# Optimization experiments

Hardware: AMD Instinct MI355X
Metric: run time of the kernel (lower is better)

## Reference

```python
import jax, jax.numpy as jnp
import numpy as np

N_GROUPS = 32  # getGroupSize(.) assumed -> channels // 8 (or //24 for 3*ch) == 32 for ch=256
HEADS = 4


def group_norm(x, gamma, beta, groups=N_GROUPS, eps=1e-5):
    n, c = x.shape
    xg = x.reshape(n, groups, c // groups)
    mu = xg.mean(-1, keepdims=True)
    var = xg.var(-1, keepdims=True)
    xn = ((xg - mu) * jax.lax.rsqrt(var + eps)).reshape(n, c)
    return xn * gamma + beta


def setup_inputs():
    key = jax.random.key(0)
    N, E, CH, HID = 2000, 16000, 256, 256
    ks = jax.random.split(key, 24)

    def w(k, shape, s=0.02):
        return (jax.random.normal(k, shape) * s).astype(jnp.float32)

    inp = {
        'x': jax.random.normal(ks[0], (N, CH), jnp.float32),
        'edge_index': jax.random.randint(ks[1], (2, E), 0, N),
        'edge_attr': jax.random.normal(ks[2], (E, CH), jnp.float32),
        # edge_mlp: GN(3ch)+ReLU -> Linear(3ch,hid) -> GN(hid)+ReLU -> Linear(hid,ch)
        'gn_e1_g': jnp.ones((3 * CH,), jnp.float32), 'gn_e1_b': jnp.zeros((3 * CH,), jnp.float32),
        'We1': w(ks[3], (3 * CH, HID)), 'be1': jnp.zeros((HID,), jnp.float32),
        'gn_e2_g': jnp.ones((HID,), jnp.float32), 'gn_e2_b': jnp.zeros((HID,), jnp.float32),
        'We2': w(ks[4], (HID, CH)), 'be2': jnp.zeros((CH,), jnp.float32),
        # actN: GN(ch)+ReLU
        'gn_n_g': jnp.ones((CH,), jnp.float32), 'gn_n_b': jnp.zeros((CH,), jnp.float32),
        # multi-head attention projections
        'Wq': w(ks[5], (CH, CH)), 'bq': jnp.zeros((CH,), jnp.float32),
        'Wk': w(ks[6], (CH, CH)), 'bk': jnp.zeros((CH,), jnp.float32),
        'Wv': w(ks[7], (CH, CH)), 'bv': jnp.zeros((CH,), jnp.float32),
        'Wo': w(ks[8], (CH, CH)), 'bo': jnp.zeros((CH,), jnp.float32),
        # node_mlp: Linear(2ch,hid) -> GN(hid)+ReLU -> Linear(hid,ch)
        'Wn1': w(ks[9], (2 * CH, HID)), 'bn1': jnp.zeros((HID,), jnp.float32),
        'gn_n2_g': jnp.ones((HID,), jnp.float32), 'gn_n2_b': jnp.zeros((HID,), jnp.float32),
        'Wn2': w(ks[10], (HID, CH)), 'bn2': jnp.zeros((CH,), jnp.float32),
    }
    return inp


def reference(x, edge_index, edge_attr,
              gn_e1_g, gn_e1_b, We1, be1, gn_e2_g, gn_e2_b, We2, be2,
              gn_n_g, gn_n_b, Wq, bq, Wk, bk, Wv, bv, Wo, bo,
              Wn1, bn1, gn_n2_g, gn_n2_b, Wn2, bn2):
    row, col = edge_index[0], edge_index[1]
    N, ch = x.shape
    E = edge_attr.shape[0]
    dk = ch // HEADS

    # ---- edge model: cat(src, tgt, e) -> GN/ReLU -> Lin -> GN/ReLU -> Lin (+res) ----
    e_in = jnp.concatenate([x[row], x[col], edge_attr], axis=1)  # [E, 3ch]
    h = jax.nn.relu(group_norm(e_in, gn_e1_g, gn_e1_b))
    h = h @ We1 + be1
    h = jax.nn.relu(group_norm(h, gn_e2_g, gn_e2_b))
    e_out = h @ We2 + be2 + edge_attr  # [E, ch]

    # ---- node model: dense-masked MHA, queries=nodes, keys/values=edges ----
    mask = jnp.zeros((N, E), x.dtype).at[col, jnp.arange(E)].set(1.0)  # scatter adjacency
    q = (x @ Wq + bq).reshape(N, HEADS, dk)
    k = (e_out @ Wk + bk).reshape(E, HEADS, dk)
    v = (e_out @ Wv + bv).reshape(E, HEADS, dk)
    scores = jnp.einsum('nhd,ehd->hne', q, k) / jnp.sqrt(jnp.float32(dk))  # [H, N, E]
    scores = jnp.where(mask[None] > 0, scores, jnp.float32(-1e9))
    attn = jax.nn.softmax(scores, axis=-1)
    g = jnp.einsum('hne,ehd->nhd', attn, v).reshape(N, ch) @ Wo + bo  # [N, ch]

    xa = jax.nn.relu(group_norm(x, gn_n_g, gn_n_b))
    h = jnp.concatenate([xa, g], axis=1) @ Wn1 + bn1  # thinker='cat'
    h = jax.nn.relu(group_norm(h, gn_n2_g, gn_n2_b))
    n_out = h @ Wn2 + bn2 + x  # residual

    return n_out, e_out
```

## Files before the change

### kernel.cpp

```cpp
#include <hip/hip_runtime.h>
#include <hip/hip_bf16.h>
#include <stdint.h>
#include <math.h>

#define CH 256

typedef __attribute__((ext_vector_type(8)))  short short8;
typedef __attribute__((ext_vector_type(16))) short short16;
typedef __attribute__((ext_vector_type(4)))  float f32x4;

#define GL2LDS16(g, l) __builtin_amdgcn_global_load_lds(                       \
    (const __attribute__((address_space(1))) void*)(g),                        \
    (__attribute__((address_space(3))) void*)(l), 16, 0, 0)

__device__ inline short f2bf(float f) {
    __hip_bfloat16 h = __float2bfloat16(f);
    short s;
    __builtin_memcpy(&s, &h, 2);
    return s;
}

__device__ inline float bf2f(short s) {
    unsigned u = ((unsigned)(unsigned short)s) << 16;
    float f;
    __builtin_memcpy(&f, &u, 4);
    return f;
}

__device__ inline float warp_sum64(float v) {
    v += __shfl_xor(v, 32, 64);
    v += __shfl_xor(v, 16, 64);
    v += __shfl_xor(v, 8, 64);
    v += __shfl_xor(v, 4, 64);
    v += __shfl_xor(v, 2, 64);
    v += __shfl_xor(v, 1, 64);
    return v;
}

__device__ inline float warp_max64(float v) {
    v = fmaxf(v, __shfl_xor(v, 32, 64));
    v = fmaxf(v, __shfl_xor(v, 16, 64));
    v = fmaxf(v, __shfl_xor(v, 8, 64));
    v = fmaxf(v, __shfl_xor(v, 4, 64));
    v = fmaxf(v, __shfl_xor(v, 2, 64));
    v = fmaxf(v, __shfl_xor(v, 1, 64));
    return v;
}

struct GArgs {
    const short* A; const short* Bt; const float* bias; const float* res;
    float* C; short* Cbf;
    const float* gamma; const float* beta; float* vbar;
    int M, K, Nc, ldc, coff;
    const short* A2; const short* Bt2; const float* bias2; short* Cbf2;
    int M2, Nc2, y_split;
    const int* coli;
    int* cursor; int* elist;
    const int* counts; int* offsets; int Nn;
};

template <int BM, int BN, int EPI, int DUAL, int VB, int FILL,
          int SCAN = 0, int PAN2 = 0, int XSWZ = 0>
__global__ __launch_bounds__(256) void mfma_gemm(GArgs g)
{
    constexpr int BK = 64;
    constexpr int HM = BM / 2, HN = BN / 2;
    constexpr int FM = HM / 16, FN = HN / 16;
    constexpr int PA = BM / 32;
    constexpr int PB = BN / 32;
    constexpr int NP2 = PAN2 ? 2 : 1;
    __shared__ short As[BM * BK];
    __shared__ short Bs[NP2 * BN * BK];

    const short* A = g.A; const short* Bt = g.Bt;
    const float* bias = g.bias; const float* res = g.res;
    float* C = g.C; short* Cbf = g.Cbf;
    int M = g.M, ldc = g.ldc, co = g.coff;
    const int K = g.K;
    int by = blockIdx.y, bx = blockIdx.x;

    if constexpr (SCAN) {
        if (by == (int)gridDim.y - 1) {
            const int t0 = threadIdx.x;
            if (bx == 0) {
                int* ss = (int*)As;
                int base8 = t0 * 8;
                int loc[8]; int srun = 0;
                #pragma unroll
                for (int j = 0; j < 8; j++) {
                    int idx = base8 + j;
                    int c = (idx < g.Nn) ? g.counts[idx] : 0;
                    loc[j] = srun; srun += c;
                }
                ss[t0] = srun;
                __syncthreads();
                for (int off = 1; off < 256; off <<= 1) {
                    int v = (t0 >= off) ? ss[t0 - off] : 0;
                    __syncthreads();
                    ss[t0] += v;
                    __syncthreads();
                }
                int excl = (t0 > 0) ? ss[t0 - 1] : 0;
                #pragma unroll
                for (int j = 0; j < 8; j++) {
                    int idx = base8 + j;
                    if (idx < g.Nn) {
                        int v = excl + loc[j];
                        g.offsets[idx] = v;
                        g.cursor[idx]  = v;
                    }
                }
                if (t0 == 255) g.offsets[g.Nn] = ss[255];
            }
            return;
        }
    }

    bool qrole = false;
    if constexpr (DUAL) {
        if (by >= g.y_split) {
            by -= g.y_split;
            if (bx * BN >= g.Nc2) return;
            qrole = true;
            A = g.A2; Bt = g.Bt2; bias = g.bias2; Cbf = g.Cbf2;
            C = nullptr; res = nullptr;
            M = g.M2; ldc = g.Nc2; co = 0;
        }
    }

    if constexpr (XSWZ) {
        if (!qrole) {
            int h = by * 4 + bx;
            int lby = (h >> 5) * 8 + (h & 7);
            if (lby * BM >= M) return;
            by = lby;
            bx = (h >> 3) & 3;
        }
    }

    const int t = threadIdx.x;
    const int wave = t >> 6, lane = t & 63;
    const int q = lane >> 4, l16 = lane & 15;
    const int row0 = by * BM;
    const int col0 = bx * BN;
    const int wm = wave & 1, wn = wave >> 1;

    if constexpr (FILL) {
        if (!qrole && bx == 0 && t < BM) {
            int rg = row0 + t;
            if (rg < M) {
                int c = g.coli[rg];
                int p = atomicAdd(&g.cursor[c], 1);
                g.elist[p] = rg;
            }
        }
    }

    f32x4 acc[NP2][FM][FN];
    #pragma unroll
    for (int p2 = 0; p2 < NP2; p2++)
        #pragma unroll
        for (int i = 0; i < FM; i++)
            #pragma unroll
            for (int j = 0; j < FN; j++) acc[p2][i][j] = (f32x4){0.f, 0.f, 0.f, 0.f};

    for (int k0 = 0; k0 < K; k0 += BK) {
        #pragma unroll
        for (int p = 0; p < PA; p++) {
            int chunk = p * 256 + t;
            int r = chunk >> 3;
            int cs = (((chunk & 7) ^ (r & 7)) * 8);
            int gr = row0 + r; if (gr >= M) gr = M - 1;
            const short* gsrc = A + (size_t)gr * K + k0 + cs;
            short* ldst = &As[(p * 256 + wave * 64) * 8];
            GL2LDS16(gsrc, ldst);
        }
        #pragma unroll
        for (int p2 = 0; p2 < NP2; p2++) {
            if (!(PAN2 && p2 == 1 && qrole)) {
                #pragma unroll
                for (int p = 0; p < PB; p++) {
                    int chunk = p * 256 + t;
                    int r = chunk >> 3;
                    int cs = (((chunk & 7) ^ (r & 7)) * 8);
                    const short* gsrc = Bt + (size_t)(col0 + p2 * 256 + r) * K + k0 + cs;
                    short* ldst = &Bs[p2 * BN * BK + (p * 256 + wave * 64) * 8];
                    GL2LDS16(gsrc, ldst);
                }
            }
        }
        __syncthreads();
        #pragma unroll
        for (int ks = 0; ks < 2; ks++) {
            short8 af[FM];
            #pragma unroll
            for (int mi = 0; mi < FM; mi++) {
                int R = wm * HM + mi * 16 + l16;
                int slot = ((ks * 4 + q) ^ (R & 7)) * 8;
                af[mi] = *(const short8*)&As[R * BK + slot];
            }
            #pragma unroll
            for (int p2 = 0; p2 < NP2; p2++) {
                if (!(PAN2 && p2 == 1 && qrole)) {
                    short8 bfr[FN];
                    #pragma unroll
                    for (int ni = 0; ni < FN; ni++) {
                        int R = wn * HN + ni * 16 + l16;
                        int slot = ((ks * 4 + q) ^ (R & 7)) * 8;
                        bfr[ni] = *(const short8*)&Bs[p2 * BN * BK + R * BK + slot];
                    }
                    #pragma unroll
                    for (int mi = 0; mi < FM; mi++)
                        #pragma unroll
                        for (int ni = 0; ni < FN; ni++)
                            acc[p2][mi][ni] = __builtin_amdgcn_mfma_f32_16x16x32_bf16(
                                af[mi], bfr[ni], acc[p2][mi][ni], 0, 0, 0);
                }
            }
        }
        __syncthreads();
    }

    #pragma unroll
    for (int p2 = 0; p2 < NP2; p2++) {
        if (PAN2 && p2 == 1 && qrole) continue;
        #pragma unroll
        for (int ni = 0; ni < FN; ni++) {
            int cg = col0 + p2 * 256 + wn * HN + ni * 16 + l16;
            float bv = bias[cg];
            if constexpr (EPI == 1) {
                float ga = g.gamma[cg], be = g.beta[cg];
                #pragma unroll
                for (int mi = 0; mi < FM; mi++) {
                    #pragma unroll
                    for (int r = 0; r < 4; r++) {
                        float v = acc[p2][mi][ni][r] + bv;
                        float s = v, sq = v * v;
                        s += __shfl_xor(s, 1, 64);  sq += __shfl_xor(sq, 1, 64);
                        s += __shfl_xor(s, 2, 64);  sq += __shfl_xor(sq, 2, 64);
                        s += __shfl_xor(s, 4, 64);  sq += __shfl_xor(sq, 4, 64);
                        float mean = s * 0.125f;
                        float var = sq * 0.125f - mean * mean;
                        float o = fmaxf((v - mean) * rsqrtf(var + 1e-5f) * ga + be, 0.f);
                        int rg = row0 + wm * HM + mi * 16 + q * 4 + r;
                        if (rg < M) Cbf[(size_t)rg * ldc + co + cg] = f2bf(o);
                    }
                }
            } else {
                #pragma unroll
                for (int mi = 0; mi < FM; mi++) {
                    #pragma unroll
                    for (int r = 0; r < 4; r++) {
                        int rg = row0 + wm * HM + mi * 16 + q * 4 + r;
                        if (rg < M) {
                            float v = acc[p2][mi][ni][r] + bv;
                            if (res) v += res[(size_t)rg * ldc + co + cg];
                            if (C)   C[(size_t)rg * ldc + co + cg] = v;
                            if (Cbf) Cbf[(size_t)rg * ldc + co + cg] = f2bf(v);
                        }
                    }
                }
                if constexpr (VB) {
                    bool vpanel = PAN2 ? (p2 == 1) : (!qrole && cg >= 256);
                    if (vpanel) {
                        float part = 0.f;
                        #pragma unroll
                        for (int mi = 0; mi < FM; mi++)
                            #pragma unroll
                            for (int r = 0; r < 4; r++) {
                                int rg = row0 + wm * HM + mi * 16 + q * 4 + r;
                                if (rg < M) part += acc[p2][mi][ni][r] + bv;
                            }
                        part += __shfl_xor(part, 16, 64);
                        part += __shfl_xor(part, 32, 64);
                        if (q == 0) atomicAdd(&g.vbar[cg - 256], part);
                    }
                }
            }
        }
    }
}

struct PrepPack {
    const float* wsrc[7];
    short* wdst[7];
    int wK[7];
    int wE[7];
    int wstart[7];
    int NW, NF, NP;
    const float* Wo; const float* Wn1s; const float* bo; const float* bn1;
    short* Wn1t; float* b2f;
    const float* x;
    short* x_bf;
    short* cat_bf;
    float2* xs;
    const float* gng;
    const float* gnb;
    float* vbar;
    const float* bk;
    const float* bv;
    float* bkv;
    int* counts;
    int N;
};

__global__ __launch_bounds__(256) void prep_kernel(PrepPack p)
{
    int bid = blockIdx.x;
    int t = threadIdx.x;
    if (bid < p.NW) {
        int m = 0;
        #pragma unroll
        for (int i = 1; i < 7; i++) if (bid >= p.wstart[i]) m = i;
        int k0 = (bid - p.wstart[m]) * 16;
        const float* src = p.wsrc[m];
        short16 o;
        #pragma unroll
        for (int j = 0; j < 16; j++) o[j] = f2bf(src[(size_t)(k0 + j) * 256 + t]);
        *(short16*)(p.wdst[m] + (size_t)t * p.wK[m] + k0) = o;
        return;
    }
    if (bid < p.NW + p.NF) {
        int c = bid - p.NW;
        __shared__ float colv[256];
        __shared__ float red[4];
        colv[t] = p.Wn1s[(size_t)(256 + t) * 256 + c];
        __syncthreads();
        const float* wrow = p.Wo + (size_t)t * 256;
        float acc = 0.f;
        #pragma unroll 4
        for (int j = 0; j < 256; j++) acc += wrow[j] * colv[j];
        p.Wn1t[(size_t)c * 512 + 256 + t] = f2bf(acc);
        float bvp = p.bo[t] * colv[t];
        bvp = warp_sum64(bvp);
        if ((t & 63) == 0) red[t >> 6] = bvp;
        __syncthreads();
        if (t == 0) p.b2f[c] = p.bn1[c] + red[0] + red[1] + red[2] + red[3];
        return;
    }
    if (bid >= p.NW + p.NF + p.NP) {
        int i = (bid - p.NW - p.NF - p.NP) * 256 + t;
        if (i < p.N) p.counts[i] = 0;
        return;
    }
    int pb = bid - p.NW - p.NF;
    if (pb == 0) {
        p.vbar[t] = 0.f;
        p.bkv[t] = p.bk[t];
        p.bkv[256 + t] = p.bv[t];
    }
    int r = pb * 8 + (t >> 5);
    int g = t & 31;
    if (r >= p.N) return;
    size_t xb = (size_t)r * CH + g * 8;
    float4 a = *(const float4*)&p.x[xb];
    float4 b = *(const float4*)&p.x[xb + 4];
    short8 xr;
    xr[0] = f2bf(a.x); xr[1] = f2bf(a.y); xr[2] = f2bf(a.z); xr[3] = f2bf(a.w);
    xr[4] = f2bf(b.x); xr[5] = f2bf(b.y); xr[6] = f2bf(b.z); xr[7] = f2bf(b.w);
    *(short8*)&p.x_bf[xb] = xr;
    float s  = a.x + a.y + a.z + a.w + b.x + b.y + b.z + b.w;
    float s2 = a.x*a.x + a.y*a.y + a.z*a.z + a.w*a.w
             + b.x*b.x + b.y*b.y + b.z*b.z + b.w*b.w;
    p.xs[(size_t)r * 32 + g] = make_float2(s, s2);
    float m = s * 0.125f;
    float var = s2 * 0.125f - m * m;
    float rsd = rsqrtf(var + 1e-5f);
    float4 g0 = *(const float4*)&p.gng[g * 8];
    float4 g1 = *(const float4*)&p.gng[g * 8 + 4];
    float4 b0 = *(const float4*)&p.gnb[g * 8];
    float4 b1 = *(const float4*)&p.gnb[g * 8 + 4];
    short8 o;
    o[0] = f2bf(fmaxf((a.x - m) * rsd * g0.x + b0.x, 0.f));
    o[1] = f2bf(fmaxf((a.y - m) * rsd * g0.y + b0.y, 0.f));
    o[2] = f2bf(fmaxf((a.z - m) * rsd * g0.z + b0.z, 0.f));
    o[3] = f2bf(fmaxf((a.w - m) * rsd * g0.w + b0.w, 0.f));
    o[4] = f2bf(fmaxf((b.x - m) * rsd * g1.x + b1.x, 0.f));
    o[5] = f2bf(fmaxf((b.y - m) * rsd * g1.y + b1.y, 0.f));
    o[6] = f2bf(fmaxf((b.z - m) * rsd * g1.z + b1.z, 0.f));
    o[7] = f2bf(fmaxf((b.w - m) * rsd * g1.w + b1.w, 0.f));
    *(short8*)&p.cat_bf[(size_t)r * (2 * CH) + g * 8] = o;
}

__global__ __launch_bounds__(256) void estats_kernel(
    const float* __restrict__ eattr, const int* __restrict__ rowi,
    const int* __restrict__ coli, const float2* __restrict__ xs,
    const short* __restrict__ x_bf,
    const float* __restrict__ g1v, const float* __restrict__ b1v,
    short* __restrict__ e1n, int* __restrict__ counts, int E)
{
    __shared__ float2 ea[8][32];
    __shared__ float2 musr[8][32];
    int t = threadIdx.x;
    int slot = t >> 5, g = t & 31;
    int e = blockIdx.x * 8 + slot;
    float4 a = *(const float4*)&eattr[(size_t)e * CH + g * 8];
    float4 b = *(const float4*)&eattr[(size_t)e * CH + g * 8 + 4];
    float s  = a.x + a.y + a.z + a.w + b.x + b.y + b.z + b.w;
    float s2 = a.x*a.x + a.y*a.y + a.z*a.z + a.w*a.w
             + b.x*b.x + b.y*b.y + b.z*b.z + b.w*b.w;
    ea[slot][g] = make_float2(s, s2);
    int r = rowi[e], c = coli[e];
    if (g == 0) atomicAdd(&counts[c], 1);
    __syncthreads();
    float S = 0.f, S2 = 0.f;
    #pragma unroll
    for (int j = 0; j < 3; j++) {
        int b3 = 3 * g + j;
        int src = b3 >> 5, idx = b3 & 31;
        float2 v;
        if (src == 0)      v = xs[(size_t)r * 32 + idx];
        else if (src == 1) v = xs[(size_t)c * 32 + idx];
        else               v = ea[slot][idx];
        S += v.x; S2 += v.y;
    }
    float m = S * (1.f / 24.f);
    float var = S2 * (1.f / 24.f) - m * m;
    musr[slot][g] = make_float2(m, rsqrtf(var + 1e-5f));
    __syncthreads();
    #pragma unroll
    for (int seg = 0; seg < 3; seg++) {
        int pos = seg * 256 + g * 8;
        float2 ms = musr[slot][pos / 24];
        float4 ga  = *(const float4*)&g1v[pos];
        float4 ga2 = *(const float4*)&g1v[pos + 4];
        float4 gb  = *(const float4*)&b1v[pos];
        float4 gb2 = *(const float4*)&b1v[pos + 4];
        float v0, v1, v2, v3, v4, v5, v6, v7;
        if (seg == 2) {
            v0 = a.x; v1 = a.y; v2 = a.z; v3 = a.w;
            v4 = b.x; v5 = b.y; v6 = b.z; v7 = b.w;
        } else {
            const short* srow = x_bf + (size_t)(seg == 0 ? r : c) * CH + g * 8;
            short8 v8 = *(const short8*)srow;
            v0 = bf2f(v8[0]); v1 = bf2f(v8[1]); v2 = bf2f(v8[2]); v3 = bf2f(v8[3]);
            v4 = bf2f(v8[4]); v5 = bf2f(v8[5]); v6 = bf2f(v8[6]); v7 = bf2f(v8[7]);
        }
        short8 o;
        o[0] = f2bf(fmaxf((v0 - ms.x) * ms.y * ga.x  + gb.x,  0.f));
        o[1] = f2bf(fmaxf((v1 - ms.x) * ms.y * ga.y  + gb.y,  0.f));
        o[2] = f2bf(fmaxf((v2 - ms.x) * ms.y * ga.z  + gb.z,  0.f));
        o[3] = f2bf(fmaxf((v3 - ms.x) * ms.y * ga.w  + gb.w,  0.f));
        o[4] = f2bf(fmaxf((v4 - ms.x) * ms.y * ga2.x + gb2.x, 0.f));
        o[5] = f2bf(fmaxf((v5 - ms.x) * ms.y * ga2.y + gb2.y, 0.f));
        o[6] = f2bf(fmaxf((v6 - ms.x) * ms.y * ga2.z + gb2.z, 0.f));
        o[7] = f2bf(fmaxf((v7 - ms.x) * ms.y * ga2.w + gb2.w, 0.f));
        *(short8*)&e1n[(size_t)e * 768 + pos] = o;
    }
}

__global__ __launch_bounds__(256) void attn_kernel(
    const short* __restrict__ qb, const short* __restrict__ kvb,
    const int* __restrict__ offsets, const int* __restrict__ elist,
    const float* __restrict__ vbar, short* __restrict__ gout, int N, int E)
{
    __shared__ int eidx[64];
    __shared__ float scl[4 * 64];
    int n = blockIdx.x;
    int wave = threadIdx.x >> 6;
    int lane = threadIdx.x & 63;
    int s0 = offsets[n], s1 = offsets[n + 1];
    float q0 = bf2f(qb[(size_t)n * CH + lane]);
    float q1 = bf2f(qb[(size_t)n * CH + 64 + lane]);
    float q2 = bf2f(qb[(size_t)n * CH + 128 + lane]);
    float q3 = bf2f(qb[(size_t)n * CH + 192 + lane]);
    float out = 0.f, m = -INFINITY, l = 0.f;
    for (int base = s0; base < s1; base += 64) {
        int cn = s1 - base; if (cn > 64) cn = 64;
        if (wave == 0 && lane < cn) eidx[lane] = elist[base + lane];
        __syncthreads();
        for (int j = wave; j < cn; j += 4) {
            int e = eidx[j];
            const short* kr = kvb + (size_t)e * 512;
            float d0 = warp_sum64(q0 * bf2f(kr[lane]));
            float d1 = warp_sum64(q1 * bf2f(kr[64 + lane]));
            float d2 = warp_sum64(q2 * bf2f(kr[128 + lane]));
            float d3 = warp_sum64(q3 * bf2f(kr[192 + lane]));
            if (lane == 0) {
                scl[j]       = d0 * 0.125f;
                scl[64 + j]  = d1 * 0.125f;
                scl[128 + j] = d2 * 0.125f;
                scl[192 + j] = d3 * 0.125f;
            }
        }
        __syncthreads();
        float s = (lane < cn) ? scl[wave * 64 + lane] : -INFINITY;
        float mc = warp_max64(s);
        float nm = fmaxf(m, mc);
        float scale = __expf(m - nm);
        float pp = (lane < cn) ? __expf(s - nm) : 0.f;
        float ps = warp_sum64(pp);
        l = l * scale + ps;
        out *= scale;
        m = nm;
        for (int i = 0; i < cn; i++) {
            float pi = __shfl(pp, i, 64);
            int ei = eidx[i];
            out += pi * bf2f(kvb[(size_t)ei * 512 + 256 + wave * 64 + lane]);
        }
        __syncthreads();
    }
    float res;
    if (s1 > s0) res = out / l;
    else         res = vbar[wave * 64 + lane] * (1.f / (float)E);
    gout[(size_t)n * 512 + wave * 64 + lane] = f2bf(res);
}

extern "C" void kernel_launch(void* const* d_in, const int* in_sizes, int n_in,
                              void* d_out, int out_size, void* d_ws, size_t ws_size,
                              hipStream_t stream)
{
    const float* x       = (const float*)d_in[0];
    const int*   ei      = (const int*)d_in[1];
    const float* eattr   = (const float*)d_in[2];
    const float* gn_e1_g = (const float*)d_in[3];
    const float* gn_e1_b = (const float*)d_in[4];
    const float* We1     = (const float*)d_in[5];
    const float* be1     = (const float*)d_in[6];
    const float* gn_e2_g = (const float*)d_in[7];
    const float* gn_e2_b = (const float*)d_in[8];
    const float* We2     = (const float*)d_in[9];
    const float* be2     = (const float*)d_in[10];
    const float* gn_n_g  = (const float*)d_in[11];
    const float* gn_n_b  = (const float*)d_in[12];
    const float* Wq      = (const float*)d_in[13];
    const float* bq      = (const float*)d_in[14];
    const float* Wk      = (const float*)d_in[15];
    const float* bk      = (const float*)d_in[16];
    const float* Wv      = (const float*)d_in[17];
    const float* bv      = (const float*)d_in[18];
    const float* Wo      = (const float*)d_in[19];
    const float* bo      = (const float*)d_in[20];
    const float* Wn1     = (const float*)d_in[21];
    const float* bn1     = (const float*)d_in[22];
    const float* gn_n2_g = (const float*)d_in[23];
    const float* gn_n2_b = (const float*)d_in[24];
    const float* Wn2     = (const float*)d_in[25];
    const float* bn2     = (const float*)d_in[26];

    const int N = in_sizes[0] / CH;
    const int E = in_sizes[2] / CH;

    float* nout = (float*)d_out;
    float* eout = (float*)d_out + (size_t)N * CH;

    char* base = (char*)d_ws;
    short* kv_bf  = (short*)base; base += (size_t)E * 512 * 2;
    short* h2_bf  = (short*)base; base += (size_t)E * CH * 2;
    short* eo_bf  = (short*)base; base += (size_t)E * CH * 2;
    short* e1n    = (short*)base; base += (size_t)E * 768 * 2;
    short* q_bf   = (short*)base; base += (size_t)N * CH * 2;
    short* g_bf   = (short*)base; base += (size_t)N * CH * 2;
    short* cat_bf = (short*)base; base += (size_t)N * 2 * CH * 2;
    short* hn_bf  = (short*)base; base += (size_t)N * CH * 2;
    short* x_bf   = (short*)base; base += (size_t)N * CH * 2;
    float2* xs    = (float2*)base; base += (size_t)N * 32 * 8;
    float* vbar   = (float*)base; base += 1024;
    float* bkv    = (float*)base; base += 2048;
    float* b2f    = (float*)base; base += 1024;
    short* We1t = (short*)base; base += (size_t)768 * 256 * 2;
    short* We2t = (short*)base; base += (size_t)256 * 256 * 2;
    short* Wqt  = (short*)base; base += (size_t)256 * 256 * 2;
    short* Wkvt = (short*)base; base += (size_t)512 * 256 * 2;
    short* Wn1t = (short*)base; base += (size_t)512 * 256 * 2;
    short* Wn2t = (short*)base; base += (size_t)256 * 256 * 2;
    int* counts  = (int*)base;
    int* offsets = counts + N;
    int* cursor  = offsets + (N + 1) + 3;
    int* elist   = cursor + N;

    const int* rowi = ei;
    const int* coli = ei + E;
    (void)g_bf;

    dim3 blk(256);

    PrepPack pp;
    const float* wsrc[7] = {We1, We2, Wq, Wk, Wv, Wn1, Wn2};
    short* wdst[7] = {We1t, We2t, Wqt, Wkvt, Wkvt + (size_t)256 * 256, Wn1t, Wn2t};
    const int wKd[7] = {768, 256, 256, 256, 256, 512, 256};
    const int wEd[7] = {768, 256, 256, 256, 256, 256, 256};
    int acc = 0;
    for (int i = 0; i < 7; i++) {
        pp.wsrc[i] = wsrc[i]; pp.wdst[i] = wdst[i];
        pp.wK[i] = wKd[i]; pp.wE[i] = wEd[i];
        pp.wstart[i] = acc; acc += wEd[i] / 16;
    }
    pp.NW = acc;
    pp.NF = 256;
    pp.NP = (N + 7) / 8;
    pp.Wo = Wo; pp.Wn1s = Wn1; pp.bo = bo; pp.bn1 = bn1;
    pp.Wn1t = Wn1t; pp.b2f = b2f;
    pp.x = x; pp.x_bf = x_bf; pp.cat_bf = cat_bf; pp.xs = xs;
    pp.gng = gn_n_g; pp.gnb = gn_n_b;
    pp.vbar = vbar; pp.bk = bk; pp.bv = bv; pp.bkv = bkv;
    pp.counts = counts; pp.N = N;
    int nzero = (N + 255) / 256;
    prep_kernel<<<pp.NW + pp.NF + pp.NP + nzero, blk, 0, stream>>>(pp);

    estats_kernel<<<E / 8, blk, 0, stream>>>(eattr, rowi, coli, xs, x_bf,
                                             gn_e1_g, gn_e1_b, e1n, counts, E);

    GArgs ga = {};
    ga.A = e1n; ga.Bt = We1t; ga.bias = be1; ga.Cbf = h2_bf;
    ga.gamma = gn_e2_g; ga.beta = gn_e2_b;
    ga.M = E; ga.K = 3 * CH; ga.Nc = CH; ga.ldc = CH; ga.coff = 0;
    ga.counts = counts; ga.offsets = offsets; ga.cursor = cursor; ga.Nn = N;
    mfma_gemm<64, 64, 1, 0, 0, 0, 1, 0, 1><<<dim3(4, 257), blk, 0, stream>>>(ga);

    ga = {};
    ga.A = h2_bf; ga.Bt = We2t; ga.bias = be2; ga.res = eattr;
    ga.C = eout; ga.Cbf = eo_bf;
    ga.M = E; ga.K = CH; ga.Nc = CH; ga.ldc = CH; ga.coff = 0;
    mfma_gemm<64, 64, 0, 0, 0, 0, 0, 0, 1><<<dim3(4, 256), blk, 0, stream>>>(ga);

    ga = {};
    ga.A = eo_bf; ga.Bt = Wkvt; ga.bias = bkv; ga.Cbf = kv_bf; ga.vbar = vbar;
    ga.M = E; ga.K = CH; ga.Nc = 512; ga.ldc = 512; ga.coff = 0;
    ga.A2 = x_bf; ga.Bt2 = Wqt; ga.bias2 = bq; ga.Cbf2 = q_bf;
    ga.M2 = N; ga.Nc2 = CH; ga.y_split = 256;
    ga.coli = coli; ga.cursor = cursor; ga.elist = elist;
    mfma_gemm<64, 64, 0, 1, 1, 1, 0, 1, 1><<<dim3(4, 256 + (N + 63) / 64), blk, 0, stream>>>(ga);

    attn_kernel<<<N, blk, 0, stream>>>(q_bf, kv_bf, offsets, elist, vbar,
                                       cat_bf + 256, N, E);

    ga = {};
    ga.A = cat_bf; ga.Bt = Wn1t; ga.bias = b2f; ga.Cbf = hn_bf;
    ga.gamma = gn_n2_g; ga.beta = gn_n2_b;
    ga.M = N; ga.K = 2 * CH; ga.Nc = CH; ga.ldc = CH; ga.coff = 0;
    mfma_gemm<32, 64, 1, 0, 0, 0><<<dim3(4, (N + 31) / 32), blk, 0, stream>>>(ga);

    ga = {};
    ga.A = hn_bf; ga.Bt = Wn2t; ga.bias = bn2; ga.res = x; ga.C = nout;
    ga.M = N; ga.K = CH; ga.Nc = CH; ga.ldc = CH; ga.coff = 0;
    mfma_gemm<32, 64, 0, 0, 0, 0><<<dim3(4, (N + 31) / 32), blk, 0, stream>>>(ga);
}
```

Measured before the change: 230.5 us.

## Move Wo·Wn1 weight folding from prep kernel into estats kernel tail blocks

The fold of Wo into the lower half of Wn1 (and of bo into the fused bias) moves out of the 256 extra prep-kernel blocks and into 65 extra blocks appended to the edge-stats kernel. Each new block computes four output columns using Wo rows staged in shared memory and coalesced reads of Wn1, replacing the old per-column dot products that read Wo rows with strided access. This shortens the prep kernel's critical path and overlaps the fold with the edge-stats work. The writes to Wn1t are now scattered 2-byte stores.

```diff
diff --git a/kernel.cpp b/kernel.cpp
--- a/kernel.cpp
+++ b/kernel.cpp
@@ -285,11 +285,8 @@
     const float* wsrc[7];
     short* wdst[7];
     int wK[7];
-    int wE[7];
     int wstart[7];
-    int NW, NF, NP;
-    const float* Wo; const float* Wn1s; const float* bo; const float* bn1;
-    short* Wn1t; float* b2f;
+    int NW, NP;
     const float* x;
     short* x_bf;
     short* cat_bf;
@@ -320,30 +317,12 @@
         *(short16*)(p.wdst[m] + (size_t)t * p.wK[m] + k0) = o;
         return;
     }
-    if (bid < p.NW + p.NF) {
-        int c = bid - p.NW;
-        __shared__ float colv[256];
-        __shared__ float red[4];
-        colv[t] = p.Wn1s[(size_t)(256 + t) * 256 + c];
-        __syncthreads();
-        const float* wrow = p.Wo + (size_t)t * 256;
-        float acc = 0.f;
-        #pragma unroll 4
-        for (int j = 0; j < 256; j++) acc += wrow[j] * colv[j];
-        p.Wn1t[(size_t)c * 512 + 256 + t] = f2bf(acc);
-        float bvp = p.bo[t] * colv[t];
-        bvp = warp_sum64(bvp);
-        if ((t & 63) == 0) red[t >> 6] = bvp;
-        __syncthreads();
-        if (t == 0) p.b2f[c] = p.bn1[c] + red[0] + red[1] + red[2] + red[3];
-        return;
-    }
-    if (bid >= p.NW + p.NF + p.NP) {
-        int i = (bid - p.NW - p.NF - p.NP) * 256 + t;
+    if (bid >= p.NW + p.NP) {
+        int i = (bid - p.NW - p.NP) * 256 + t;
         if (i < p.N) p.counts[i] = 0;
         return;
     }
-    int pb = bid - p.NW - p.NF;
+    int pb = bid - p.NW;
     if (pb == 0) {
         p.vbar[t] = 0.f;
         p.bkv[t] = p.bk[t];
@@ -387,11 +366,43 @@
     const int* __restrict__ coli, const float2* __restrict__ xs,
     const short* __restrict__ x_bf,
     const float* __restrict__ g1v, const float* __restrict__ b1v,
-    short* __restrict__ e1n, int* __restrict__ counts, int E)
+    short* __restrict__ e1n, int* __restrict__ counts,
+    const float* __restrict__ Wo, const float* __restrict__ bo,
+    const float* __restrict__ bn1, const float* __restrict__ Wn1raw,
+    short* __restrict__ Wn1t, float* __restrict__ b2f, int nE8, int E)
 {
+    int t = threadIdx.x;
+    if ((int)blockIdx.x >= nE8) {
+        int fb = blockIdx.x - nE8;
+        __shared__ float wo[4][256];
+        if (fb < 64) {
+            #pragma unroll
+            for (int i = 0; i < 4; i++) wo[i][t] = Wo[(size_t)(fb * 4 + i) * 256 + t];
+        } else {
+            wo[0][t] = bo[t];
+        }
+        __syncthreads();
+        float a0 = 0.f, a1 = 0.f, a2 = 0.f, a3 = 0.f;
+        if (fb < 64) {
+            for (int j = 0; j < 256; j++) {
+                float wn = Wn1raw[(size_t)(256 + j) * 256 + t];
+                a0 += wo[0][j] * wn; a1 += wo[1][j] * wn;
+                a2 += wo[2][j] * wn; a3 += wo[3][j] * wn;
+            }
+            int k0 = fb * 4;
+            Wn1t[(size_t)t * 512 + 256 + k0]     = f2bf(a0);
+            Wn1t[(size_t)t * 512 + 256 + k0 + 1] = f2bf(a1);
+            Wn1t[(size_t)t * 512 + 256 + k0 + 2] = f2bf(a2);
+            Wn1t[(size_t)t * 512 + 256 + k0 + 3] = f2bf(a3);
+        } else {
+            for (int j = 0; j < 256; j++)
+                a0 += wo[0][j] * Wn1raw[(size_t)(256 + j) * 256 + t];
+            b2f[t] = bn1[t] + a0;
+        }
+        return;
+    }
     __shared__ float2 ea[8][32];
     __shared__ float2 musr[8][32];
-    int t = threadIdx.x;
     int slot = t >> 5, g = t & 31;
     int e = blockIdx.x * 8 + slot;
     float4 a = *(const float4*)&eattr[(size_t)e * CH + g * 8];
@@ -582,24 +593,23 @@
     const int wEd[7] = {768, 256, 256, 256, 256, 256, 256};
     int acc = 0;
     for (int i = 0; i < 7; i++) {
-        pp.wsrc[i] = wsrc[i]; pp.wdst[i] = wdst[i];
-        pp.wK[i] = wKd[i]; pp.wE[i] = wEd[i];
+        pp.wsrc[i] = wsrc[i]; pp.wdst[i] = wdst[i]; pp.wK[i] = wKd[i];
         pp.wstart[i] = acc; acc += wEd[i] / 16;
     }
     pp.NW = acc;
-    pp.NF = 256;
     pp.NP = (N + 7) / 8;
-    pp.Wo = Wo; pp.Wn1s = Wn1; pp.bo = bo; pp.bn1 = bn1;
-    pp.Wn1t = Wn1t; pp.b2f = b2f;
     pp.x = x; pp.x_bf = x_bf; pp.cat_bf = cat_bf; pp.xs = xs;
     pp.gng = gn_n_g; pp.gnb = gn_n_b;
     pp.vbar = vbar; pp.bk = bk; pp.bv = bv; pp.bkv = bkv;
     pp.counts = counts; pp.N = N;
     int nzero = (N + 255) / 256;
-    prep_kernel<<<pp.NW + pp.NF + pp.NP + nzero, blk, 0, stream>>>(pp);
-
-    estats_kernel<<<E / 8, blk, 0, stream>>>(eattr, rowi, coli, xs, x_bf,
-                                             gn_e1_g, gn_e1_b, e1n, counts, E);
+    prep_kernel<<<pp.NW + pp.NP + nzero, blk, 0, stream>>>(pp);
+
+    int nE8 = E / 8;
+    estats_kernel<<<nE8 + 65, blk, 0, stream>>>(eattr, rowi, coli, xs, x_bf,
+                                                gn_e1_g, gn_e1_b, e1n, counts,
+                                                Wo, bo, bn1, Wn1, Wn1t, b2f,
+                                                nE8, E);
 
     GArgs ga = {};
     ga.A = e1n; ga.Bt = We1t; ga.bias = be1; ga.Cbf = h2_bf;
```

Measured after the change: 229.8 us. Within noise of the previous version (-0.3%).
